# Optimization experiments

Measured on AMD Instinct MI355X. Metric: run time of the kernel, lower is better.

The kernel has to match this reference:

```python
import jax, jax.numpy as jnp
import numpy as np
from jax import lax

N_SEEDS = 16
N_SAMPS = 32
IN_C = 3
HID = [32, 64, 64]
K = 3
H = W = 64
EPS = 1e-5


def _uniform(key, shape, bound):
    return jax.random.uniform(key, shape, jnp.float32, -bound, bound)


def setup_inputs() -> dict:
    key = jax.random.key(0)
    keys = jax.random.split(key, 32)
    inp = {"x": jax.random.normal(keys[0], (N_SEEDS, N_SAMPS, IN_C, H, W), jnp.float32)}
    c_in = IN_C
    ki = 1
    for li, c_out in enumerate(HID, start=1):
        fan_in = c_in * K * K
        # kaiming_uniform with a=sqrt(5): gain=sqrt(2/(1+5))=sqrt(1/3); bound=sqrt(3)*gain/sqrt(fan)=1/sqrt(fan)
        wb = 1.0 / np.sqrt(fan_in)
        inp[f"w{li}"] = _uniform(keys[ki], (N_SEEDS * c_out, c_in, K, K), wb); ki += 1
        inp[f"b{li}"] = _uniform(keys[ki], (N_SEEDS * c_out,), wb); ki += 1
        inp[f"g{li}"] = jnp.ones((N_SEEDS * c_out,), jnp.float32)
        inp[f"be{li}"] = jnp.zeros((N_SEEDS * c_out,), jnp.float32)
        c_in = c_out
    return inp


def _layer(h, w, b, g, be):
    # grouped conv: groups = N_SEEDS, OIHW weights, NCHW data, stride 1, pad 1
    h = lax.conv_general_dilated(
        h, w, window_strides=(1, 1), padding=((1, 1), (1, 1)),
        feature_group_count=N_SEEDS,
        dimension_numbers=("NCHW", "OIHW", "NCHW"))
    h = h + b[None, :, None, None]
    # BatchNorm2d, training mode: batch statistics over (N, H, W), biased variance
    mean = jnp.mean(h, axis=(0, 2, 3))
    var = jnp.var(h, axis=(0, 2, 3))
    h = (h - mean[None, :, None, None]) * (g / jnp.sqrt(var + EPS))[None, :, None, None] + be[None, :, None, None]
    return jax.nn.relu(h)


def reference(x, w1, b1, g1, be1, w2, b2, g2, be2, w3, b3, g3, be3):
    S, N, C, Hh, Ww = x.shape  # (n_seeds, n_samps, C, H, W)
    h = jnp.swapaxes(x, 0, 1).reshape(N, S * C, Hh, Ww)
    h = _layer(h, w1, b1, g1, be1)
    h = _layer(h, w2, b2, g2, be2)
    h = _layer(h, w3, b3, g3, be3)
    c_out = HID[-1]
    h = h.reshape(N, S, c_out, Hh, Ww)
    return jnp.swapaxes(h, 0, 1)  # (n_seeds, n_samps, C_out, H, W)
```

## Files before the change

### kernel.cpp

```cpp
#include <hip/hip_runtime.h>
#include <cstddef>
#include <cstdint>

typedef __attribute__((ext_vector_type(8))) _Float16 half8;
typedef __attribute__((ext_vector_type(4))) float f32x4;
typedef _Float16 half_t;

#define NS 16
#define NN 32

static const size_t OFF_H1P = 0;
static const size_t OFF_H2P = 138412032ull;
static const size_t OFF_ZR1 = OFF_H2P + 276824064ull;
static const size_t OFF_ZR2 = OFF_ZR1 + 67584ull;
static const size_t OFF_WT1 = OFF_ZR2 + 135168ull;
static const size_t OFF_WT2 = OFF_WT1 + 55296ull;
static const size_t OFF_WT3 = OFF_WT2 + 589824ull;
static const size_t OFF_SUMS = OFF_WT3 + 1179648ull;
static const size_t OFF_PRM = OFF_SUMS + 20480ull;
static const size_t OFF_TH  = OFF_PRM + 30720ull;

static __device__ __forceinline__ half8 sr8(half8 v, half8 t) {
    half8 r = v + t;
    half8 z = {};
#if defined(__has_builtin) && __has_builtin(__builtin_elementwise_max)
    return __builtin_elementwise_max(r, z);
#else
#pragma unroll
    for (int j = 0; j < 8; ++j) r[j] = r[j] > (_Float16)0 ? r[j] : (_Float16)0;
    return r;
#endif
}

__global__ __launch_bounds__(256) void transform1_k(
    const float* __restrict__ w1, float* __restrict__ wt1)
{
    int idx = blockIdx.x * 256 + threadIdx.x;
    if (idx >= 13824) return;
    int o = idx & 31, tap = (idx >> 5) % 9, ic = (idx / 288) % 3, s = idx / 864;
    wt1[idx] = w1[((s * 32 + o) * 3 + ic) * 9 + tap];
}

__global__ __launch_bounds__(256) void wtrans2_k(
    const float* __restrict__ w2, const float* __restrict__ a1, half_t* __restrict__ wt2)
{
    int idx = blockIdx.x * 256 + threadIdx.x;
    if (idx >= 294912) return;
    int ic = idx & 31, oc = (idx >> 5) & 63, tap = (idx >> 11) % 9, s = idx / 18432;
    wt2[idx] = (half_t)(w2[((s * 64 + oc) * 32 + ic) * 9 + tap] * a1[s * 32 + ic]);
}

__global__ __launch_bounds__(256) void wtrans3_k(
    const float* __restrict__ w3, const float* __restrict__ a2, half_t* __restrict__ wt3)
{
    int idx = blockIdx.x * 256 + threadIdx.x;
    if (idx >= 589824) return;
    int ic = idx & 63, oc = (idx >> 6) & 63, tap = (idx >> 12) % 9, s = idx / 36864;
    wt3[idx] = (half_t)(w3[((s * 64 + oc) * 64 + ic) * 9 + tap] * a2[s * 64 + ic]);
}

__global__ __launch_bounds__(256) void conv1_k(
    const float* __restrict__ x, const float* __restrict__ wt1,
    const float* __restrict__ b1, half_t* __restrict__ h1p,
    float* __restrict__ sums1)
{
    __shared__ float smem[8512];
    float* xt = smem;
    float* bounce = smem;
    float* statsl = smem + 8448;
    const int tile = blockIdx.x, s = blockIdx.y, n = blockIdx.z;
    const int tx = tile & 3, ty = tile >> 2, tid = threadIdx.x;

    for (int i = tid; i < 972; i += 256) {
        int ic = i / 324, rem = i - ic * 324;
        int py = rem / 18, px = rem - py * 18;
        int gy = ty * 16 + py - 1, gx = tx * 16 + px - 1;
        float v = 0.f;
        if ((unsigned)gy < 64u && (unsigned)gx < 64u)
            v = x[(size_t)(((s * NN + n) * 3 + ic) * 64 + gy) * 64 + gx];
        xt[i] = v;
    }
    if (tid < 64) statsl[tid] = 0.f;
    __syncthreads();

    const int px = tid & 15, py = tid >> 4;
    float acc[32];
#pragma unroll
    for (int o = 0; o < 32; ++o) acc[o] = 0.f;
#pragma unroll
    for (int ic = 0; ic < 3; ++ic)
#pragma unroll
        for (int ky = 0; ky < 3; ++ky)
#pragma unroll
            for (int kx = 0; kx < 3; ++kx) {
                float v = xt[ic * 324 + (py + ky) * 18 + px + kx];
                const float* wp = wt1 + ((s * 3 + ic) * 9 + ky * 3 + kx) * 32;
#pragma unroll
                for (int o = 0; o < 32; ++o) acc[o] = fmaf(wp[o], v, acc[o]);
            }
    const float* bp = b1 + s * 32;
#pragma unroll
    for (int o = 0; o < 32; ++o) acc[o] += bp[o];

    const int gy1 = ty * 16 + py, gxp = tx * 16 + px + 1;
    half8* dst = (half8*)(h1p + (size_t)(n * NS + s) * 135168 + (size_t)(gy1 * 66 + gxp) * 32);
#pragma unroll
    for (int k = 0; k < 4; ++k) {
        half8 v8;
#pragma unroll
        for (int j = 0; j < 8; ++j) v8[j] = (half_t)acc[k * 8 + j];
        dst[k] = v8;
    }
    __syncthreads();
#pragma unroll
    for (int o = 0; o < 32; ++o) bounce[tid * 33 + o] = acc[o];
    __syncthreads();
    {
        const int oc = tid & 31, grp = tid >> 5;
        float s1 = 0.f, s2 = 0.f;
#pragma unroll 4
        for (int j = 0; j < 32; ++j) {
            float v = bounce[(grp * 32 + j) * 33 + oc];
            s1 += v; s2 += v * v;
        }
        atomicAdd(&statsl[oc * 2], s1);
        atomicAdd(&statsl[oc * 2 + 1], s2);
    }
    __syncthreads();
    if (tid < 64)
        atomicAdd(&sums1[(s * 32 + (tid >> 1)) * 2 + (tid & 1)], statsl[tid]);
}

__global__ void bnparam_k(const float* __restrict__ sums, const float* __restrict__ g,
                          const float* __restrict__ be, float* __restrict__ a,
                          float* __restrict__ b, float* __restrict__ t,
                          half_t* __restrict__ th, int C)
{
    int ch = blockIdx.x * 256 + threadIdx.x;
    if (ch >= C) return;
    const float inv = 1.f / 131072.f;
    float mean = sums[ch * 2] * inv;
    float var = sums[ch * 2 + 1] * inv - mean * mean;
    float sc = g[ch] * rsqrtf(var + 1e-5f);
    a[ch] = sc;
    float bb = be[ch] - mean * sc;
    b[ch] = bb;
    float tt = bb / sc;
    t[ch] = tt;
    th[ch] = (half_t)tt;
}

__global__ __launch_bounds__(256) void padfill_k(
    half_t* __restrict__ img, half_t* __restrict__ zrow, const float* __restrict__ t,
    int C, int c8shift, long imgstride, int rowstride, long tot_cols, long tot)
{
    long idx = (long)blockIdx.x * 256 + threadIdx.x;
    if (idx >= tot) return;
    const int nc8m = (1 << c8shift) - 1;
    if (idx < tot_cols) {
        int c8 = (int)idx & nc8m; long r = idx >> c8shift;
        int side = (int)r & 1; r >>= 1;
        int y = (int)r & 63; r >>= 6;
        int si = (int)(r & 15); int ni = (int)(r >> 4);
        half8 q;
#pragma unroll
        for (int j = 0; j < 8; ++j) q[j] = (half_t)(-(t[si * C + c8 * 8 + j] + 1.0f));
        *(half8*)(img + (long)(ni * NS + si) * imgstride + (long)y * rowstride +
                  (side ? 65 : 0) * C + c8 * 8) = q;
    } else {
        long r2 = idx - tot_cols;
        int c8 = (int)r2 & nc8m; r2 >>= c8shift;
        int xx = (int)(r2 % 66); int si = (int)(r2 / 66);
        half8 q;
#pragma unroll
        for (int j = 0; j < 8; ++j) q[j] = (half_t)(-(t[si * C + c8 * 8 + j] + 1.0f));
        *(half8*)(zrow + ((long)(si * 66 + xx)) * C + c8 * 8) = q;
    }
}

__device__ __forceinline__ void loadB2(half8 bf[4], const half_t* wb, int tap, int l15, int g) {
#pragma unroll
    for (int nt = 0; nt < 4; ++nt)
        bf[nt] = *(const half8*)(wb + (tap * 64 + nt * 16 + l15) * 32 + g * 8);
}

__device__ __forceinline__ void comp2(f32x4 acc[4][4], const half8 bf[4], const char* smem,
                                      int tap, int wv, int l15, int g) {
    const int ky = tap / 3, kx = tap - ky * 3;
#pragma unroll
    for (int mt = 0; mt < 4; ++mt) {
        int p = (wv * 4 + mt + ky) * 18 + l15 + kx;
        half8 av = *(const half8*)(smem + p * 80 + g * 16);
#pragma unroll
        for (int nt = 0; nt < 4; ++nt)
            acc[mt][nt] = __builtin_amdgcn_mfma_f32_16x16x32_f16(av, bf[nt], acc[mt][nt], 0, 0, 0);
    }
}

__global__ __launch_bounds__(256, 3) void conv2_k(
    const half_t* __restrict__ h1p, const half_t* __restrict__ zr1,
    const half_t* __restrict__ wt2, const float* __restrict__ b2,
    const half_t* __restrict__ th1, half_t* __restrict__ h2p,
    float* __restrict__ sums2)
{
    __shared__ __align__(16) char smem[37376];
    float* statsl = (float*)(smem + 36864);
    const int tile = blockIdx.x, s = blockIdx.y, n = blockIdx.z;
    const int tx = tile & 3, ty = tile >> 2, tid = threadIdx.x;
    const int l = tid & 63, wv = tid >> 6, l15 = l & 15, g = l >> 4;
    if (tid < 128) statsl[tid] = 0.f;

    const half_t* wb = wt2 + (size_t)s * 18432;
    half8 bfa[4], bfb[4];
    loadB2(bfa, wb, 0, l15, g);

    const half_t* img = h1p + (size_t)(n * NS + s) * 135168;
    const half_t* zrow = zr1 + s * 2112;
    const int j = tid & 3;
    const half8 tshj = *(const half8*)(th1 + s * 32 + j * 8);
    for (int i = tid; i < 1296; i += 256) {
        int p = i >> 2;
        int py = p / 18, pxx = p - py * 18;
        int gy = ty * 16 + py - 1;
        const half_t* rp = ((unsigned)gy < 64u) ? (img + (size_t)gy * 2112) : zrow;
        half8 v = sr8(*(const half8*)(rp + (tx * 16 + pxx) * 32 + j * 8), tshj);
        *(half8*)(smem + p * 80 + j * 16) = v;
    }
    __syncthreads();

    f32x4 acc[4][4];
#pragma unroll
    for (int mt = 0; mt < 4; ++mt)
#pragma unroll
        for (int nt = 0; nt < 4; ++nt) acc[mt][nt] = (f32x4){0.f, 0.f, 0.f, 0.f};

#pragma unroll
    for (int tap = 0; tap < 9; ++tap) {
        if (tap & 1) {
            if (tap < 8) loadB2(bfa, wb, tap + 1, l15, g);
            comp2(acc, bfb, smem, tap, wv, l15, g);
        } else {
            if (tap < 8) loadB2(bfb, wb, tap + 1, l15, g);
            comp2(acc, bfa, smem, tap, wv, l15, g);
        }
    }

    float s1a[4], s2a[4];
#pragma unroll
    for (int nt = 0; nt < 4; ++nt) {
        float bias = b2[s * 64 + nt * 16 + l15];
        float s1 = 0.f, s2 = 0.f;
#pragma unroll
        for (int mt = 0; mt < 4; ++mt)
#pragma unroll
            for (int r = 0; r < 4; ++r) {
                float v = acc[mt][nt][r] + bias;
                acc[mt][nt][r] = v;
                s1 += v; s2 += v * v;
            }
        s1 += __shfl_xor(s1, 16); s1 += __shfl_xor(s1, 32);
        s2 += __shfl_xor(s2, 16); s2 += __shfl_xor(s2, 32);
        s1a[nt] = s1; s2a[nt] = s2;
    }
    if (l < 16) {
#pragma unroll
        for (int nt = 0; nt < 4; ++nt) {
            atomicAdd(&statsl[(nt * 16 + l15) * 2], s1a[nt]);
            atomicAdd(&statsl[(nt * 16 + l15) * 2 + 1], s2a[nt]);
        }
    }
    __syncthreads();

    half_t* obuf = (half_t*)smem;
#pragma unroll
    for (int mt = 0; mt < 4; ++mt)
#pragma unroll
        for (int nt = 0; nt < 4; ++nt)
#pragma unroll
            for (int r = 0; r < 4; ++r)
                obuf[((wv * 4 + mt) * 16 + g * 4 + r) * 72 + nt * 16 + l15] = (half_t)acc[mt][nt][r];
    __syncthreads();

    half_t* img2 = h2p + (size_t)(n * NS + s) * 270336;
    for (int i = tid; i < 2048; i += 256) {
        int p = i >> 3, cc = i & 7;
        int y = ty * 16 + (p >> 4), xp = tx * 16 + (p & 15) + 1;
        *(half8*)(img2 + (size_t)y * 4224 + xp * 64 + cc * 8) = *(const half8*)(obuf + p * 72 + cc * 8);
    }
    if (tid < 128)
        atomicAdd(&sums2[(s * 64 + (tid >> 1)) * 2 + (tid & 1)], statsl[tid]);
}

__device__ __forceinline__ void loadB3(half8 bf[2][2], const half_t* wb, int tap,
                                       int och, int l15, int g) {
#pragma unroll
    for (int nt = 0; nt < 2; ++nt) {
        const half_t* r = wb + (tap * 64 + och * 32 + nt * 16 + l15) * 64 + g * 8;
        bf[nt][0] = *(const half8*)(r);
        bf[nt][1] = *(const half8*)(r + 32);
    }
}

__device__ __forceinline__ void comp3(f32x4 acc[4][2], const half8 bf[2][2], const char* smem,
                                      int tap, int wy, int l15, int g) {
    const int ky = tap / 3, kx = tap - ky * 3;
#pragma unroll
    for (int mt = 0; mt < 4; ++mt) {
        int p = (wy + ky) * 66 + mt * 16 + l15 + kx;
        int base = p * 128, sw = (p & 7) << 4;
        half8 a0 = *(const half8*)(smem + base + ((g * 16) ^ sw));
        half8 a1 = *(const half8*)(smem + base + ((64 + g * 16) ^ sw));
#pragma unroll
        for (int nt = 0; nt < 2; ++nt) {
            acc[mt][nt] = __builtin_amdgcn_mfma_f32_16x16x32_f16(a0, bf[nt][0], acc[mt][nt], 0, 0, 0);
            acc[mt][nt] = __builtin_amdgcn_mfma_f32_16x16x32_f16(a1, bf[nt][1], acc[mt][nt], 0, 0, 0);
        }
    }
}

__global__ __launch_bounds__(512, 4) void conv3_k(
    const half_t* __restrict__ h2p, const half_t* __restrict__ zr2,
    const half_t* __restrict__ wt3, const float* __restrict__ b3,
    const half_t* __restrict__ th2, float* __restrict__ out,
    float* __restrict__ sums3)
{
    __shared__ __align__(16) char smem[51200];
    float* statsl = (float*)(smem + 50688);
    const int ty = blockIdx.x, s = blockIdx.y, n = blockIdx.z;
    const int tid = threadIdx.x;
    const int l = tid & 63, w = tid >> 6, l15 = l & 15, g = l >> 4;
    const int wy = w & 3, och = w >> 2;
    if (tid < 128) statsl[tid] = 0.f;

    const half_t* wb = wt3 + (size_t)s * 36864;
    half8 bfa[2][2], bfb[2][2];
    loadB3(bfa, wb, 0, och, l15, g);

    const half_t* img = h2p + (size_t)(n * NS + s) * 270336;
    const half_t* zrow = zr2 + s * 4224;
    const int j = tid & 7;
    const half8 tshj = *(const half8*)(th2 + s * 64 + j * 8);
    for (int i = tid; i < 3168; i += 512) {
        int p = i >> 3;
        int row = p / 66, col = p - row * 66;
        int gy = ty * 4 + row - 1;
        const half_t* rp = ((unsigned)gy < 64u) ? (img + (size_t)gy * 4224) : zrow;
        half8 v = sr8(*(const half8*)(rp + col * 64 + j * 8), tshj);
        *(half8*)(smem + p * 128 + ((j * 16) ^ ((p & 7) << 4))) = v;
    }
    __syncthreads();

    f32x4 acc[4][2];
#pragma unroll
    for (int mt = 0; mt < 4; ++mt)
#pragma unroll
        for (int nt = 0; nt < 2; ++nt) acc[mt][nt] = (f32x4){0.f, 0.f, 0.f, 0.f};

#pragma unroll
    for (int tap = 0; tap < 9; ++tap) {
        if (tap & 1) {
            if (tap < 8) loadB3(bfa, wb, tap + 1, och, l15, g);
            comp3(acc, bfb, smem, tap, wy, l15, g);
        } else {
            if (tap < 8) loadB3(bfb, wb, tap + 1, och, l15, g);
            comp3(acc, bfa, smem, tap, wy, l15, g);
        }
    }

    float s1a[2], s2a[2];
#pragma unroll
    for (int nt = 0; nt < 2; ++nt) {
        float bias = b3[s * 64 + och * 32 + nt * 16 + l15];
        float s1 = 0.f, s2 = 0.f;
#pragma unroll
        for (int mt = 0; mt < 4; ++mt)
#pragma unroll
            for (int r = 0; r < 4; ++r) {
                float v = acc[mt][nt][r] + bias;
                acc[mt][nt][r] = v;
                s1 += v; s2 += v * v;
            }
        s1 += __shfl_xor(s1, 16); s1 += __shfl_xor(s1, 32);
        s2 += __shfl_xor(s2, 16); s2 += __shfl_xor(s2, 32);
        s1a[nt] = s1; s2a[nt] = s2;
    }
    if (l < 16) {
#pragma unroll
        for (int nt = 0; nt < 2; ++nt) {
            atomicAdd(&statsl[(och * 32 + nt * 16 + l15) * 2], s1a[nt]);
            atomicAdd(&statsl[(och * 32 + nt * 16 + l15) * 2 + 1], s2a[nt]);
        }
    }

    const int gy = ty * 4 + wy;
#pragma unroll
    for (int mt = 0; mt < 4; ++mt)
#pragma unroll
        for (int nt = 0; nt < 2; ++nt) {
            int c = och * 32 + nt * 16 + l15;
            *(f32x4*)(out + ((size_t)((s * NN + n) * 64 + c) * 64 + gy) * 64 + mt * 16 + g * 4) = acc[mt][nt];
        }
    __syncthreads();
    if (tid < 128)
        atomicAdd(&sums3[(s * 64 + (tid >> 1)) * 2 + (tid & 1)], statsl[tid]);
}

__global__ __launch_bounds__(256) void final_k(float* __restrict__ out,
                                               const float* __restrict__ a3,
                                               const float* __restrict__ b3p)
{
    size_t i = ((size_t)blockIdx.x * 256 + threadIdx.x) * 4;
    int ch = (int)((i >> 12) & 63) + (int)(i >> 23) * 64;
    float sc = a3[ch], sh = b3p[ch];
    f32x4 v = *(f32x4*)(out + i);
#pragma unroll
    for (int r = 0; r < 4; ++r) v[r] = fmaxf(fmaf(sc, v[r], sh), 0.f);
    *(f32x4*)(out + i) = v;
}

extern "C" void kernel_launch(void* const* d_in, const int* in_sizes, int n_in,
                              void* d_out, int out_size, void* d_ws, size_t ws_size,
                              hipStream_t stream)
{
    const float* x   = (const float*)d_in[0];
    const float* w1  = (const float*)d_in[1];
    const float* b1  = (const float*)d_in[2];
    const float* g1  = (const float*)d_in[3];
    const float* be1 = (const float*)d_in[4];
    const float* w2  = (const float*)d_in[5];
    const float* b2  = (const float*)d_in[6];
    const float* g2  = (const float*)d_in[7];
    const float* be2 = (const float*)d_in[8];
    const float* w3  = (const float*)d_in[9];
    const float* b3  = (const float*)d_in[10];
    const float* g3  = (const float*)d_in[11];
    const float* be3 = (const float*)d_in[12];

    char* ws = (char*)d_ws;
    half_t* h1p = (half_t*)(ws + OFF_H1P);
    half_t* h2p = (half_t*)(ws + OFF_H2P);
    half_t* zr1 = (half_t*)(ws + OFF_ZR1);
    half_t* zr2 = (half_t*)(ws + OFF_ZR2);
    float*  wt1 = (float*)(ws + OFF_WT1);
    half_t* wt2 = (half_t*)(ws + OFF_WT2);
    half_t* wt3 = (half_t*)(ws + OFF_WT3);
    float*  sums = (float*)(ws + OFF_SUMS);
    float *s1v = sums, *s2v = sums + 1024, *s3v = sums + 3072;
    float*  prm = (float*)(ws + OFF_PRM);
    float *a1 = prm,        *b1p = prm + 512,  *t1 = prm + 1024;
    float *a2 = prm + 1536, *b2p = prm + 2560, *t2 = prm + 3584;
    float *a3 = prm + 4608, *b3p = prm + 5632, *t3 = prm + 6656;
    half_t* th = (half_t*)(ws + OFF_TH);
    half_t *th1 = th, *th2 = th + 512, *th3 = th + 1536;
    float* out = (float*)d_out;

    hipMemsetAsync(ws + OFF_SUMS, 0, 20480, stream);
    transform1_k<<<54, 256, 0, stream>>>(w1, wt1);
    dim3 grid(16, 16, 32);
    conv1_k<<<grid, 256, 0, stream>>>(x, wt1, b1, h1p, s1v);
    bnparam_k<<<2, 256, 0, stream>>>(s1v, g1, be1, a1, b1p, t1, th1, 512);
    padfill_k<<<1041, 256, 0, stream>>>(h1p, zr1, t1, 32, 2, 135168L, 2112, 262144L, 266368L);
    wtrans2_k<<<1152, 256, 0, stream>>>(w2, a1, wt2);
    conv2_k<<<grid, 256, 0, stream>>>(h1p, zr1, wt2, b2, th1, h2p, s2v);
    bnparam_k<<<4, 256, 0, stream>>>(s2v, g2, be2, a2, b2p, t2, th2, 1024);
    padfill_k<<<2081, 256, 0, stream>>>(h2p, zr2, t2, 64, 3, 270336L, 4224, 524288L, 532736L);
    wtrans3_k<<<2304, 256, 0, stream>>>(w3, a2, wt3);
    dim3 grid3(16, 16, 32);
    conv3_k<<<grid3, 512, 0, stream>>>(h2p, zr2, wt3, b3, th2, out, s3v);
    bnparam_k<<<4, 256, 0, stream>>>(s3v, g3, be3, a3, b3p, t3, th3, 1024);
    final_k<<<131072, 256, 0, stream>>>(out, a3, b3p);
}
```

Baseline: 877.0 us.

## Store conv3 output as fp16 intermediate and split-stage the halo load

```diff
diff --git a/kernel.cpp b/kernel.cpp
--- a/kernel.cpp
+++ b/kernel.cpp
@@ -3,6 +3,7 @@
 #include <cstdint>
 
 typedef __attribute__((ext_vector_type(8))) _Float16 half8;
+typedef __attribute__((ext_vector_type(4))) _Float16 half4;
 typedef __attribute__((ext_vector_type(4))) float f32x4;
 typedef _Float16 half_t;
 
@@ -10,8 +11,8 @@
 #define NN 32
 
 static const size_t OFF_H1P = 0;
-static const size_t OFF_H2P = 138412032ull;
-static const size_t OFF_ZR1 = OFF_H2P + 276824064ull;
+static const size_t OFF_H3  = 138412032ull;
+static const size_t OFF_ZR1 = 138412032ull + 276824064ull;
 static const size_t OFF_ZR2 = OFF_ZR1 + 67584ull;
 static const size_t OFF_WT1 = OFF_ZR2 + 135168ull;
 static const size_t OFF_WT2 = OFF_WT1 + 55296ull;
@@ -119,8 +120,8 @@
         const int oc = tid & 31, grp = tid >> 5;
         float s1 = 0.f, s2 = 0.f;
 #pragma unroll 4
-        for (int j = 0; j < 32; ++j) {
-            float v = bounce[(grp * 32 + j) * 33 + oc];
+        for (int jj = 0; jj < 32; ++jj) {
+            float v = bounce[(grp * 32 + jj) * 33 + oc];
             s1 += v; s2 += v * v;
         }
         atomicAdd(&statsl[oc * 2], s1);
@@ -291,37 +292,10 @@
         atomicAdd(&sums2[(s * 64 + (tid >> 1)) * 2 + (tid & 1)], statsl[tid]);
 }
 
-__device__ __forceinline__ void loadB3(half8 bf[2][2], const half_t* wb, int tap,
-                                       int och, int l15, int g) {
-#pragma unroll
-    for (int nt = 0; nt < 2; ++nt) {
-        const half_t* r = wb + (tap * 64 + och * 32 + nt * 16 + l15) * 64 + g * 8;
-        bf[nt][0] = *(const half8*)(r);
-        bf[nt][1] = *(const half8*)(r + 32);
-    }
-}
-
-__device__ __forceinline__ void comp3(f32x4 acc[4][2], const half8 bf[2][2], const char* smem,
-                                      int tap, int wy, int l15, int g) {
-    const int ky = tap / 3, kx = tap - ky * 3;
-#pragma unroll
-    for (int mt = 0; mt < 4; ++mt) {
-        int p = (wy + ky) * 66 + mt * 16 + l15 + kx;
-        int base = p * 128, sw = (p & 7) << 4;
-        half8 a0 = *(const half8*)(smem + base + ((g * 16) ^ sw));
-        half8 a1 = *(const half8*)(smem + base + ((64 + g * 16) ^ sw));
-#pragma unroll
-        for (int nt = 0; nt < 2; ++nt) {
-            acc[mt][nt] = __builtin_amdgcn_mfma_f32_16x16x32_f16(a0, bf[nt][0], acc[mt][nt], 0, 0, 0);
-            acc[mt][nt] = __builtin_amdgcn_mfma_f32_16x16x32_f16(a1, bf[nt][1], acc[mt][nt], 0, 0, 0);
-        }
-    }
-}
-
 __global__ __launch_bounds__(512, 4) void conv3_k(
     const half_t* __restrict__ h2p, const half_t* __restrict__ zr2,
     const half_t* __restrict__ wt3, const float* __restrict__ b3,
-    const half_t* __restrict__ th2, float* __restrict__ out,
+    const half_t* __restrict__ th2, half_t* __restrict__ h3,
     float* __restrict__ sums3)
 {
     __shared__ __align__(16) char smem[51200];
@@ -330,24 +304,42 @@
     const int tid = threadIdx.x;
     const int l = tid & 63, w = tid >> 6, l15 = l & 15, g = l >> 4;
     const int wy = w & 3, och = w >> 2;
+    const int ty4 = ty * 4;
     if (tid < 128) statsl[tid] = 0.f;
-
-    const half_t* wb = wt3 + (size_t)s * 36864;
-    half8 bfa[2][2], bfb[2][2];
-    loadB3(bfa, wb, 0, och, l15, g);
 
     const half_t* img = h2p + (size_t)(n * NS + s) * 270336;
     const half_t* zrow = zr2 + s * 4224;
+    const half_t* wb = wt3 + (size_t)s * 36864;
     const int j = tid & 7;
     const half8 tshj = *(const half8*)(th2 + s * 64 + j * 8);
-    for (int i = tid; i < 3168; i += 512) {
-        int p = i >> 3;
-        int row = p / 66, col = p - row * 66;
-        int gy = ty * 4 + row - 1;
-        const half_t* rp = ((unsigned)gy < 64u) ? (img + (size_t)gy * 4224) : zrow;
-        half8 v = sr8(*(const half8*)(rp + col * 64 + j * 8), tshj);
-        *(half8*)(smem + p * 128 + ((j * 16) ^ ((p & 7) << 4))) = v;
-    }
+
+    half8 sa0, sa1, sa2, sa3, sa4; int aa0, aa1, aa2, aa3, aa4;
+#define PREPA(K, ST, SL) { int idx = tid + K * 512; int p = idx >> 3; int rr = p / 66; \
+    int col = p - rr * 66; int row = ty4 - 1 + rr; bool ok = idx < 2112; \
+    const half_t* rp = ((unsigned)row < 64u) ? (img + (size_t)row * 4224) : zrow; \
+    ST = *(const half8*)(rp + col * 64 + j * 8); \
+    SL = ok ? (rr * 8448 + col * 128 + ((j * 16) ^ ((col & 7) << 4))) : -1; }
+    PREPA(0, sa0, aa0)
+    PREPA(1, sa1, aa1)
+    PREPA(2, sa2, aa2)
+    PREPA(3, sa3, aa3)
+    PREPA(4, sa4, aa4)
+#undef PREPA
+    half8 sb0, sb1, sb2; int ab0, ab1, ab2;
+#define PREPB(K, ST, SL) { int idx = tid + K * 512; int p = idx >> 3; int rr = p / 66; \
+    int col = p - rr * 66; int row = ty4 + 3 + rr; bool ok = idx < 1056; \
+    const half_t* rp = ((unsigned)row < 64u) ? (img + (size_t)row * 4224) : zrow; \
+    ST = *(const half8*)(rp + col * 64 + j * 8); \
+    SL = ok ? ((4 + rr) * 8448 + col * 128 + ((j * 16) ^ ((col & 7) << 4))) : -1; }
+    PREPB(0, sb0, ab0)
+    PREPB(1, sb1, ab1)
+    PREPB(2, sb2, ab2)
+#undef PREPB
+    if (aa0 >= 0) *(half8*)(smem + aa0) = sr8(sa0, tshj);
+    if (aa1 >= 0) *(half8*)(smem + aa1) = sr8(sa1, tshj);
+    if (aa2 >= 0) *(half8*)(smem + aa2) = sr8(sa2, tshj);
+    if (aa3 >= 0) *(half8*)(smem + aa3) = sr8(sa3, tshj);
+    if (aa4 >= 0) *(half8*)(smem + aa4) = sr8(sa4, tshj);
     __syncthreads();
 
     f32x4 acc[4][2];
@@ -356,66 +348,102 @@
 #pragma unroll
         for (int nt = 0; nt < 2; ++nt) acc[mt][nt] = (f32x4){0.f, 0.f, 0.f, 0.f};
 
-#pragma unroll
-    for (int tap = 0; tap < 9; ++tap) {
-        if (tap & 1) {
-            if (tap < 8) loadB3(bfa, wb, tap + 1, och, l15, g);
-            comp3(acc, bfb, smem, tap, wy, l15, g);
-        } else {
-            if (tap < 8) loadB3(bfb, wb, tap + 1, och, l15, g);
-            comp3(acc, bfa, smem, tap, wy, l15, g);
-        }
-    }
-
-    float s1a[2], s2a[2];
-#pragma unroll
-    for (int nt = 0; nt < 2; ++nt) {
-        float bias = b3[s * 64 + och * 32 + nt * 16 + l15];
-        float s1 = 0.f, s2 = 0.f;
-#pragma unroll
-        for (int mt = 0; mt < 4; ++mt)
-#pragma unroll
-            for (int r = 0; r < 4; ++r) {
-                float v = acc[mt][nt][r] + bias;
-                acc[mt][nt][r] = v;
-                s1 += v; s2 += v * v;
-            }
-        s1 += __shfl_xor(s1, 16); s1 += __shfl_xor(s1, 32);
-        s2 += __shfl_xor(s2, 16); s2 += __shfl_xor(s2, 32);
-        s1a[nt] = s1; s2a[nt] = s2;
-    }
-    if (l < 16) {
-#pragma unroll
-        for (int nt = 0; nt < 2; ++nt) {
-            atomicAdd(&statsl[(och * 32 + nt * 16 + l15) * 2], s1a[nt]);
-            atomicAdd(&statsl[(och * 32 + nt * 16 + l15) * 2 + 1], s2a[nt]);
-        }
-    }
-
-    const int gy = ty * 4 + wy;
+    const int UT[19] = {0,1,2,0,1,2, 3,4,5,6,7,8, 3,4,5,6,7,8, 0};
+    const int UK[19] = {0,0,0,1,1,1, 0,0,0,0,0,0, 1,1,1,1,1,1, 0};
+    half8 bfa[2], bfb[2];
+#define LW3(BF, U) { \
+    BF[0] = *(const half8*)(wb + (UT[U] * 64 + och * 32 + l15) * 64 + UK[U] * 32 + g * 8); \
+    BF[1] = *(const half8*)(wb + (UT[U] * 64 + och * 32 + 16 + l15) * 64 + UK[U] * 32 + g * 8); }
+    LW3(bfa, 0)
+#define CSTEP3(BF, U) { \
+    int tap_ = UT[U]; int ky_ = tap_ / 3, kx_ = tap_ - ky_ * 3; \
+    const char* rp_ = smem + (wy + ky_) * 8448; \
+    _Pragma("unroll") \
+    for (int mt = 0; mt < 4; ++mt) { \
+        int px = mt * 16 + l15 + kx_; \
+        int sw = (px & 7) << 4; \
+        half8 a_ = *(const half8*)(rp_ + px * 128 + ((UK[U] * 64 + g * 16) ^ sw)); \
+        acc[mt][0] = __builtin_amdgcn_mfma_f32_16x16x32_f16(a_, BF[0], acc[mt][0], 0, 0, 0); \
+        acc[mt][1] = __builtin_amdgcn_mfma_f32_16x16x32_f16(a_, BF[1], acc[mt][1], 0, 0, 0); \
+    } }
+
+    LW3(bfb, 1)  CSTEP3(bfa, 0)
+    LW3(bfa, 2)  CSTEP3(bfb, 1)
+    LW3(bfb, 3)  CSTEP3(bfa, 2)
+    LW3(bfa, 4)  CSTEP3(bfb, 3)
+    LW3(bfb, 5)  CSTEP3(bfa, 4)
+    LW3(bfa, 6)  CSTEP3(bfb, 5)
+    if (ab0 >= 0) *(half8*)(smem + ab0) = sr8(sb0, tshj);
+    if (ab1 >= 0) *(half8*)(smem + ab1) = sr8(sb1, tshj);
+    if (ab2 >= 0) *(half8*)(smem + ab2) = sr8(sb2, tshj);
+    __syncthreads();
+    LW3(bfb, 7)   CSTEP3(bfa, 6)
+    LW3(bfa, 8)   CSTEP3(bfb, 7)
+    LW3(bfb, 9)   CSTEP3(bfa, 8)
+    LW3(bfa, 10)  CSTEP3(bfb, 9)
+    LW3(bfb, 11)  CSTEP3(bfa, 10)
+    LW3(bfa, 12)  CSTEP3(bfb, 11)
+    LW3(bfb, 13)  CSTEP3(bfa, 12)
+    LW3(bfa, 14)  CSTEP3(bfb, 13)
+    LW3(bfb, 15)  CSTEP3(bfa, 14)
+    LW3(bfa, 16)  CSTEP3(bfb, 15)
+    LW3(bfb, 17)  CSTEP3(bfa, 16)
+                  CSTEP3(bfb, 17)
+#undef CSTEP3
+#undef LW3
+
+    float bias0 = b3[s * 64 + och * 32 + l15];
+    float bias1 = b3[s * 64 + och * 32 + 16 + l15];
+    float s10 = 0.f, s20 = 0.f, s11 = 0.f, s21 = 0.f;
+    const int gy = ty4 + wy;
+    half_t* hb = h3 + (size_t)((s * NN + n) * 64) * 4096;
 #pragma unroll
     for (int mt = 0; mt < 4; ++mt)
 #pragma unroll
         for (int nt = 0; nt < 2; ++nt) {
             int c = och * 32 + nt * 16 + l15;
-            *(f32x4*)(out + ((size_t)((s * NN + n) * 64 + c) * 64 + gy) * 64 + mt * 16 + g * 4) = acc[mt][nt];
+            float bias = nt ? bias1 : bias0;
+            half4 hv;
+#pragma unroll
+            for (int r = 0; r < 4; ++r) {
+                float vv = acc[mt][nt][r] + bias;
+                hv[r] = (half_t)vv;
+                if (nt) { s11 += vv; s21 += vv * vv; } else { s10 += vv; s20 += vv * vv; }
+            }
+            *(half4*)(hb + (size_t)c * 4096 + gy * 64 + mt * 16 + g * 4) = hv;
         }
+
+    s10 += __shfl_xor(s10, 16); s10 += __shfl_xor(s10, 32);
+    s20 += __shfl_xor(s20, 16); s20 += __shfl_xor(s20, 32);
+    s11 += __shfl_xor(s11, 16); s11 += __shfl_xor(s11, 32);
+    s21 += __shfl_xor(s21, 16); s21 += __shfl_xor(s21, 32);
+    if (l < 16) {
+        atomicAdd(&statsl[(och * 32 + l15) * 2], s10);
+        atomicAdd(&statsl[(och * 32 + l15) * 2 + 1], s20);
+        atomicAdd(&statsl[(och * 32 + 16 + l15) * 2], s11);
+        atomicAdd(&statsl[(och * 32 + 16 + l15) * 2 + 1], s21);
+    }
     __syncthreads();
     if (tid < 128)
         atomicAdd(&sums3[(s * 64 + (tid >> 1)) * 2 + (tid & 1)], statsl[tid]);
 }
 
 __global__ __launch_bounds__(256) void final_k(float* __restrict__ out,
+                                               const half_t* __restrict__ h3,
                                                const float* __restrict__ a3,
                                                const float* __restrict__ b3p)
 {
-    size_t i = ((size_t)blockIdx.x * 256 + threadIdx.x) * 4;
-    int ch = (int)((i >> 12) & 63) + (int)(i >> 23) * 64;
-    float sc = a3[ch], sh = b3p[ch];
-    f32x4 v = *(f32x4*)(out + i);
-#pragma unroll
-    for (int r = 0; r < 4; ++r) v[r] = fmaxf(fmaf(sc, v[r], sh), 0.f);
-    *(f32x4*)(out + i) = v;
+    const size_t stride = (size_t)gridDim.x * 256;
+    for (size_t i = (size_t)blockIdx.x * 256 + threadIdx.x; i < 33554432ull; i += stride) {
+        size_t e = i * 4;
+        int ch = (int)((e >> 12) & 63) + (int)(e >> 23) * 64;
+        float sc = a3[ch], sh = b3p[ch];
+        half4 hv = *(const half4*)(h3 + e);
+        f32x4 v;
+#pragma unroll
+        for (int r = 0; r < 4; ++r) v[r] = fmaxf(fmaf(sc, (float)hv[r], sh), 0.f);
+        *(f32x4*)(out + e) = v;
+    }
 }
 
 extern "C" void kernel_launch(void* const* d_in, const int* in_sizes, int n_in,
@@ -438,7 +466,8 @@
 
     char* ws = (char*)d_ws;
     half_t* h1p = (half_t*)(ws + OFF_H1P);
-    half_t* h2p = (half_t*)(ws + OFF_H2P);
+    half_t* h2p = (half_t*)d_out;
+    half_t* h3  = (half_t*)(ws + OFF_H3);
     half_t* zr1 = (half_t*)(ws + OFF_ZR1);
     half_t* zr2 = (half_t*)(ws + OFF_ZR2);
     float*  wt1 = (float*)(ws + OFF_WT1);
@@ -456,17 +485,17 @@
 
     hipMemsetAsync(ws + OFF_SUMS, 0, 20480, stream);
     transform1_k<<<54, 256, 0, stream>>>(w1, wt1);
-    dim3 grid(16, 16, 32);
-    conv1_k<<<grid, 256, 0, stream>>>(x, wt1, b1, h1p, s1v);
+    dim3 grid1(16, 16, 32);
+    conv1_k<<<grid1, 256, 0, stream>>>(x, wt1, b1, h1p, s1v);
     bnparam_k<<<2, 256, 0, stream>>>(s1v, g1, be1, a1, b1p, t1, th1, 512);
     padfill_k<<<1041, 256, 0, stream>>>(h1p, zr1, t1, 32, 2, 135168L, 2112, 262144L, 266368L);
     wtrans2_k<<<1152, 256, 0, stream>>>(w2, a1, wt2);
-    conv2_k<<<grid, 256, 0, stream>>>(h1p, zr1, wt2, b2, th1, h2p, s2v);
+    conv2_k<<<grid1, 256, 0, stream>>>(h1p, zr1, wt2, b2, th1, h2p, s2v);
     bnparam_k<<<4, 256, 0, stream>>>(s2v, g2, be2, a2, b2p, t2, th2, 1024);
     padfill_k<<<2081, 256, 0, stream>>>(h2p, zr2, t2, 64, 3, 270336L, 4224, 524288L, 532736L);
     wtrans3_k<<<2304, 256, 0, stream>>>(w3, a2, wt3);
     dim3 grid3(16, 16, 32);
-    conv3_k<<<grid3, 512, 0, stream>>>(h2p, zr2, wt3, b3, th2, out, s3v);
+    conv3_k<<<grid3, 512, 0, stream>>>(h2p, zr2, wt3, b3, th2, h3, s3v);
     bnparam_k<<<4, 256, 0, stream>>>(s3v, g3, be3, a3, b3p, t3, th3, 1024);
-    final_k<<<131072, 256, 0, stream>>>(out, a3, b3p);
-}
+    final_k<<<4096, 256, 0, stream>>>(out, h3, a3, b3p);
+}
```

After: 827.2 us, median of 3. 5.7% less time.
